# Kernel optimization log

Measured on AMD Instinct MI355X. Metric: run time of the kernel, lower is better.

## Reference

```python
import jax, jax.numpy as jnp
import numpy as np

N_TOKENS = 65536
HIDDEN = 1024
N_EXPERTS = 64
EPS = 1e-12  # matches F.normalize default eps
NEG_BIG = float(jnp.finfo(jnp.bfloat16).max)  # -torch.finfo(bfloat16).max sentinel


def setup_inputs() -> dict:
    key = jax.random.key(0)
    k1, k2 = jax.random.split(key)
    x = jax.random.normal(k1, (N_TOKENS, HIDDEN), dtype=jnp.float32)
    sim_matrix = jax.random.normal(k2, (HIDDEN, N_EXPERTS), dtype=jnp.float32)  # nn.Parameter(randn)
    gates = jnp.zeros((N_EXPERTS,), dtype=jnp.float32)  # nn.Parameter(zeros)
    return {"x": x, "sim_matrix": sim_matrix, "gates": gates}


def _l2norm(v, axis):
    n = jnp.sqrt(jnp.sum(v * v, axis=axis, keepdims=True))
    return v / jnp.maximum(n, EPS)


def reference(x, sim_matrix, gates):
    # cosine-similarity logits: [N, E]
    logits = jnp.matmul(_l2norm(x, -1), _l2norm(sim_matrix, 0))
    thr = jax.nn.sigmoid(gates)                      # [E]
    pre_activation_logits = logits - thr             # [N, E]
    gated = jax.nn.relu(pre_activation_logits)
    # STE: forward hard 0/1, backward identity
    hard = (gated > 0).astype(x.dtype)
    activation_mask = gated + jax.lax.stop_gradient(hard - gated)
    # topk fallback for rows with zero active experts (vectorized scatter)
    inactive = jnp.sum(hard, axis=1) == 0            # [N]
    k_fallback = N_EXPERTS // 2
    _, topk_idx = jax.lax.top_k(logits, k_fallback)  # [N, k]
    rows = jnp.arange(x.shape[0])
    fb = jnp.zeros_like(logits).at[rows[:, None], topk_idx].set(1.0)
    activation_mask = jnp.where(inactive[:, None], fb, activation_mask)
    # masked softmax over active experts
    masked = jnp.where(activation_mask > 0, gated, -NEG_BIG)
    active_expert_probs = jax.nn.softmax(masked, axis=-1)
    return active_expert_probs, pre_activation_logits, activation_mask
```

## Files before the change

### kernel.cpp

```cpp
#include <hip/hip_runtime.h>
#include <math.h>

#define N_TOK   65536
#define HID     1024
#define NEXP    64
#define EPSF    1e-12f

__global__ __launch_bounds__(256) void prep_kernel(const float* __restrict__ sim,
                                                   const float* __restrict__ gates,
                                                   float* __restrict__ ws) {
    __shared__ float partial[4][64];
    int e = threadIdx.x & 63;
    int q = threadIdx.x >> 6;
    float s = 0.f;
    for (int h = q * 256; h < q * 256 + 256; ++h) {
        float v = sim[h * NEXP + e];
        s += v * v;
    }
    partial[q][e] = s;
    __syncthreads();
    if (threadIdx.x < 64) {
        float ss = partial[0][e] + partial[1][e] + partial[2][e] + partial[3][e];
        ws[e] = 1.0f / fmaxf(sqrtf(ss), EPSF);
        ws[64 + e] = 1.0f / (1.0f + expf(-gates[e]));
    }
}

__global__ __launch_bounds__(256) void prep2n_kernel(const float* __restrict__ sim,
                                                     const float* __restrict__ ws_ro,
                                                     float* __restrict__ wn) {
    int idx = blockIdx.x * 256 + threadIdx.x;
    wn[idx] = sim[idx] * ws_ro[idx & 63];
}

__global__ __launch_bounds__(256) void gate_v9_kernel(const float* __restrict__ x,
                                                      const float* __restrict__ wn,
                                                      const float* __restrict__ prep,
                                                      float* __restrict__ out) {
    __shared__ __align__(16) float smem[8960];
    float* ss_part = smem + 8704;

    const int tid  = threadIdx.x;
    const int lane = tid & 63;
    const int wv   = tid >> 6;
    const int tg   = lane >> 3;
    const int eg   = lane & 7;
    const int e0   = eg * 8;
    const int tbase = blockIdx.x * 64;

    float* xsw = smem + wv * 2176;

    const float4* xq4 = (const float4*)(x + (size_t)(tbase + lane) * HID + wv * 256);

    float acc[8][8];
#pragma unroll
    for (int t = 0; t < 8; ++t)
#pragma unroll
        for (int e = 0; e < 8; ++e) acc[t][e] = 0.f;
    float ss = 0.f;

    {
        float4 st[4];
#pragma unroll
        for (int q = 0; q < 4; ++q) st[q] = xq4[q];
#pragma unroll
        for (int q = 0; q < 4; ++q) {
            ss = fmaf(st[q].x, st[q].x, ss);
            ss = fmaf(st[q].y, st[q].y, ss);
            ss = fmaf(st[q].z, st[q].z, ss);
            ss = fmaf(st[q].w, st[q].w, ss);
            xsw[(q * 4 + 0) * 68 + lane] = st[q].x;
            xsw[(q * 4 + 1) * 68 + lane] = st[q].y;
            xsw[(q * 4 + 2) * 68 + lane] = st[q].z;
            xsw[(q * 4 + 3) * 68 + lane] = st[q].w;
        }
    }

#define FMA8x8(XA, XB, WA, WB)                                              \
    do {                                                                    \
        const float xv_[8] = { XA.x, XA.y, XA.z, XA.w, XB.x, XB.y, XB.z, XB.w }; \
        const float wv_[8] = { WA.x, WA.y, WA.z, WA.w, WB.x, WB.y, WB.z, WB.w }; \
        _Pragma("unroll")                                                   \
        for (int t_ = 0; t_ < 8; ++t_)                                      \
            _Pragma("unroll")                                               \
            for (int e_ = 0; e_ < 8; ++e_)                                  \
                acc[t_][e_] = fmaf(xv_[t_], wv_[e_], acc[t_][e_]);          \
    } while (0)

#pragma unroll 1
    for (int c = 0; c < 16; ++c) {
        float4 st[4];
        if (c < 15) {
#pragma unroll
            for (int q = 0; q < 4; ++q) st[q] = xq4[(c + 1) * 4 + q];
        }

        const float* xb = xsw + (c & 1) * 1088;
        const float* wbase = wn + (size_t)(wv * 256 + c * 16) * NEXP + e0;

        float4 a0 = *(const float4*)(wbase);
        float4 b0 = *(const float4*)(wbase + 4);
        float4 a1 = *(const float4*)(wbase + 64);
        float4 b1 = *(const float4*)(wbase + 68);

#pragma unroll 4
        for (int k = 0; k < 16; k += 2) {
            float4 na0, nb0, na1, nb1;
            if (k + 2 < 16) {
                na0 = *(const float4*)(wbase + (k + 2) * 64);
                nb0 = *(const float4*)(wbase + (k + 2) * 64 + 4);
                na1 = *(const float4*)(wbase + (k + 3) * 64);
                nb1 = *(const float4*)(wbase + (k + 3) * 64 + 4);
            }
            const float4 xa0 = *(const float4*)&xb[k * 68 + tg * 8];
            const float4 xb0 = *(const float4*)&xb[k * 68 + tg * 8 + 4];
            const float4 xa1 = *(const float4*)&xb[(k + 1) * 68 + tg * 8];
            const float4 xb1 = *(const float4*)&xb[(k + 1) * 68 + tg * 8 + 4];
            FMA8x8(xa0, xb0, a0, b0);
            FMA8x8(xa1, xb1, a1, b1);
            a0 = na0; b0 = nb0; a1 = na1; b1 = nb1;
        }

        if (c < 15) {
            float* xn = xsw + ((c + 1) & 1) * 1088;
#pragma unroll
            for (int q = 0; q < 4; ++q) {
                ss = fmaf(st[q].x, st[q].x, ss);
                ss = fmaf(st[q].y, st[q].y, ss);
                ss = fmaf(st[q].z, st[q].z, ss);
                ss = fmaf(st[q].w, st[q].w, ss);
                xn[(q * 4 + 0) * 68 + lane] = st[q].x;
                xn[(q * 4 + 1) * 68 + lane] = st[q].y;
                xn[(q * 4 + 2) * 68 + lane] = st[q].z;
                xn[(q * 4 + 3) * 68 + lane] = st[q].w;
            }
        }
    }
#undef FMA8x8

    ss_part[wv * 64 + lane] = ss;
    __syncthreads();

    if (wv < 2) {
        float* reg = smem + wv * 4352;
#pragma unroll
        for (int j = 0; j < 8; ++j) {
            float* p = &reg[(tg * 8 + j) * 68 + e0];
            *(float4*)(p)     = make_float4(acc[j][0], acc[j][1], acc[j][2], acc[j][3]);
            *(float4*)(p + 4) = make_float4(acc[j][4], acc[j][5], acc[j][6], acc[j][7]);
        }
    }
    __syncthreads();
    if (wv >= 2) {
        float* reg = smem + (wv - 2) * 4352;
#pragma unroll
        for (int j = 0; j < 8; ++j) {
            float* p = &reg[(tg * 8 + j) * 68 + e0];
            float4 p0 = *(const float4*)(p);
            float4 p1 = *(const float4*)(p + 4);
            p0.x += acc[j][0]; p0.y += acc[j][1]; p0.z += acc[j][2]; p0.w += acc[j][3];
            p1.x += acc[j][4]; p1.y += acc[j][5]; p1.z += acc[j][6]; p1.w += acc[j][7];
            *(float4*)(p)     = p0;
            *(float4*)(p + 4) = p1;
        }
    }
    __syncthreads();

    float thr[8];
#pragma unroll
    for (int i = 0; i < 8; ++i) thr[i] = prep[64 + e0 + i];

    const size_t out_pre  = (size_t)N_TOK * NEXP;
    const size_t out_mask = 2 * (size_t)N_TOK * NEXP;
    const float* regA = smem;
    const float* regB = smem + 4352;

#pragma unroll
    for (int j = 0; j < 2; ++j) {
        const int tl = wv * 16 + tg * 2 + j;
        const int t  = tbase + tl;
        const float sst = (ss_part[tl] + ss_part[64 + tl])
                        + (ss_part[128 + tl] + ss_part[192 + tl]);
        const float inv = 1.0f / fmaxf(sqrtf(sst), EPSF);

        float4 aA0 = *(const float4*)&regA[tl * 68 + e0];
        float4 aA1 = *(const float4*)&regA[tl * 68 + e0 + 4];
        float4 aB0 = *(const float4*)&regB[tl * 68 + e0];
        float4 aB1 = *(const float4*)&regB[tl * 68 + e0 + 4];
        float logit[8] = { (aA0.x + aB0.x) * inv, (aA0.y + aB0.y) * inv,
                           (aA0.z + aB0.z) * inv, (aA0.w + aB0.w) * inv,
                           (aA1.x + aB1.x) * inv, (aA1.y + aB1.y) * inv,
                           (aA1.z + aB1.z) * inv, (aA1.w + aB1.w) * inv };
        float pre[8], gated[8];
        int active[8];
        int myact = 0;
#pragma unroll
        for (int i = 0; i < 8; ++i) {
            pre[i]   = logit[i] - thr[i];
            gated[i] = fmaxf(pre[i], 0.f);
            active[i] = pre[i] > 0.f;
            myact += active[i];
        }
        int rowact = myact;
        rowact += __shfl_xor(rowact, 1, 8);
        rowact += __shfl_xor(rowact, 2, 8);
        rowact += __shfl_xor(rowact, 4, 8);

        float probs[8], mask[8];
        if (rowact > 0) {
            float m = -INFINITY;
#pragma unroll
            for (int i = 0; i < 8; ++i) m = fmaxf(m, active[i] ? gated[i] : -INFINITY);
            m = fmaxf(m, __shfl_xor(m, 1, 8));
            m = fmaxf(m, __shfl_xor(m, 2, 8));
            m = fmaxf(m, __shfl_xor(m, 4, 8));
            float s = 0.f;
#pragma unroll
            for (int i = 0; i < 8; ++i) {
                float ev = active[i] ? expf(gated[i] - m) : 0.f;
                probs[i] = ev; s += ev;
            }
            s += __shfl_xor(s, 1, 8);
            s += __shfl_xor(s, 2, 8);
            s += __shfl_xor(s, 4, 8);
            float rs = 1.0f / s;
#pragma unroll
            for (int i = 0; i < 8; ++i) {
                probs[i] *= rs;
                mask[i] = active[i] ? 1.f : 0.f;
            }
        } else {
            unsigned key[8];
#pragma unroll
            for (int i = 0; i < 8; ++i) {
                unsigned u = __float_as_uint(logit[i]);
                key[i] = (u & 0x80000000u) ? ~u : (u | 0x80000000u);
            }
            unsigned cand = 0u;
            for (int bit = 31; bit >= 0; --bit) {
                unsigned test = cand | (1u << bit);
                int c = 0;
#pragma unroll
                for (int i = 0; i < 8; ++i) c += (key[i] >= test);
                c += __shfl_xor(c, 1, 8);
                c += __shfl_xor(c, 2, 8);
                c += __shfl_xor(c, 4, 8);
                if (c >= 32) cand = test;
            }
            int cgt = 0;
#pragma unroll
            for (int i = 0; i < 8; ++i) cgt += (key[i] > cand);
            cgt += __shfl_xor(cgt, 1, 8);
            cgt += __shfl_xor(cgt, 2, 8);
            cgt += __shfl_xor(cgt, 4, 8);
            int need_eq = 32 - cgt;

            int eqc = 0;
#pragma unroll
            for (int i = 0; i < 8; ++i) eqc += (key[i] == cand);
            int scan = eqc, tmp;
            tmp = __shfl_up(scan, 1, 8); if (eg >= 1) scan += tmp;
            tmp = __shfl_up(scan, 2, 8); if (eg >= 2) scan += tmp;
            tmp = __shfl_up(scan, 4, 8); if (eg >= 4) scan += tmp;
            int run = scan - eqc;
#pragma unroll
            for (int i = 0; i < 8; ++i) {
                int sel = (key[i] > cand) || ((key[i] == cand) && (run < need_eq));
                run += (key[i] == cand);
                mask[i]  = sel ? 1.f : 0.f;
                probs[i] = sel ? 0.03125f : 0.f;
            }
        }

        const size_t row = (size_t)t * NEXP + e0;
        *(float4*)&out[row]                = make_float4(probs[0], probs[1], probs[2], probs[3]);
        *(float4*)&out[row + 4]            = make_float4(probs[4], probs[5], probs[6], probs[7]);
        *(float4*)&out[out_pre + row]      = make_float4(pre[0], pre[1], pre[2], pre[3]);
        *(float4*)&out[out_pre + row + 4]  = make_float4(pre[4], pre[5], pre[6], pre[7]);
        *(float4*)&out[out_mask + row]     = make_float4(mask[0], mask[1], mask[2], mask[3]);
        *(float4*)&out[out_mask + row + 4] = make_float4(mask[4], mask[5], mask[6], mask[7]);
    }
}

#define TOKB    128
#define KC      64
#define XPAD    65

__global__ __launch_bounds__(256) void gate_kernel_fb(const float* __restrict__ x,
                                                      const float* __restrict__ sim,
                                                      const float* __restrict__ prep,
                                                      float* __restrict__ out) {
    __shared__ float x_lds[TOKB][XPAD];
    __shared__ float w_lds[KC][NEXP];
    __shared__ float ss_lds[TOKB];
    __shared__ float invcol[NEXP];
    __shared__ float thr_s[NEXP];

    const int tid = threadIdx.x;
    const int base_t = blockIdx.x * TOKB;

    if (tid < NEXP) { invcol[tid] = prep[tid]; thr_s[tid] = prep[64 + tid]; }
    if (tid < TOKB) ss_lds[tid] = 0.f;

    const int g_e = tid & 7;
    const int g_t = tid >> 3;
    const int e0 = g_e * 8;
    const int t0 = g_t * 4;

    const int lt = tid >> 4;
    const int lk = (tid & 15) * 4;

    float acc[4][8];
#pragma unroll
    for (int j = 0; j < 4; ++j)
#pragma unroll
        for (int i = 0; i < 8; ++i) acc[j][i] = 0.f;

    for (int kc = 0; kc < HID; kc += KC) {
        __syncthreads();
#pragma unroll
        for (int it = 0; it < 4; ++it) {
            int flat4 = it * 256 + tid;
            int k = flat4 >> 4;
            int e = (flat4 & 15) * 4;
            float4 v = *(const float4*)&sim[(size_t)(kc + k) * NEXP + e];
            v.x *= invcol[e]; v.y *= invcol[e + 1]; v.z *= invcol[e + 2]; v.w *= invcol[e + 3];
            *(float4*)&w_lds[k][e] = v;
        }
#pragma unroll
        for (int it = 0; it < 8; ++it) {
            int t = it * 16 + lt;
            float4 v = *(const float4*)&x[(size_t)(base_t + t) * HID + kc + lk];
            x_lds[t][lk + 0] = v.x; x_lds[t][lk + 1] = v.y;
            x_lds[t][lk + 2] = v.z; x_lds[t][lk + 3] = v.w;
            float s4 = v.x * v.x + v.y * v.y + v.z * v.z + v.w * v.w;
            s4 += __shfl_xor(s4, 1, 16);
            s4 += __shfl_xor(s4, 2, 16);
            s4 += __shfl_xor(s4, 4, 16);
            s4 += __shfl_xor(s4, 8, 16);
            if ((tid & 15) == 0) ss_lds[t] += s4;
        }
        __syncthreads();
#pragma unroll 8
        for (int k = 0; k < KC; ++k) {
            float x0 = x_lds[t0 + 0][k];
            float x1 = x_lds[t0 + 1][k];
            float x2 = x_lds[t0 + 2][k];
            float x3 = x_lds[t0 + 3][k];
            float4 w0 = *(const float4*)&w_lds[k][e0];
            float4 w1 = *(const float4*)&w_lds[k][e0 + 4];
            float wv[8] = { w0.x, w0.y, w0.z, w0.w, w1.x, w1.y, w1.z, w1.w };
#pragma unroll
            for (int i = 0; i < 8; ++i) {
                acc[0][i] += x0 * wv[i];
                acc[1][i] += x1 * wv[i];
                acc[2][i] += x2 * wv[i];
                acc[3][i] += x3 * wv[i];
            }
        }
    }

    const size_t out_pre  = (size_t)N_TOK * NEXP;
    const size_t out_mask = 2 * (size_t)N_TOK * NEXP;

#pragma unroll
    for (int j = 0; j < 4; ++j) {
        int t = t0 + j;
        float inv = 1.0f / fmaxf(sqrtf(ss_lds[t]), EPSF);
        float logit[8], pre[8], gated[8];
        int active[8];
        int myact = 0;
#pragma unroll
        for (int i = 0; i < 8; ++i) {
            logit[i] = acc[j][i] * inv;
            pre[i]   = logit[i] - thr_s[e0 + i];
            gated[i] = fmaxf(pre[i], 0.f);
            active[i] = pre[i] > 0.f;
            myact += active[i];
        }
        int rowact = myact;
        rowact += __shfl_xor(rowact, 1, 8);
        rowact += __shfl_xor(rowact, 2, 8);
        rowact += __shfl_xor(rowact, 4, 8);

        float probs[8], mask[8];
        if (rowact > 0) {
            float m = -INFINITY;
#pragma unroll
            for (int i = 0; i < 8; ++i) m = fmaxf(m, active[i] ? gated[i] : -INFINITY);
            m = fmaxf(m, __shfl_xor(m, 1, 8));
            m = fmaxf(m, __shfl_xor(m, 2, 8));
            m = fmaxf(m, __shfl_xor(m, 4, 8));
            float s = 0.f;
#pragma unroll
            for (int i = 0; i < 8; ++i) {
                float ev = active[i] ? expf(gated[i] - m) : 0.f;
                probs[i] = ev; s += ev;
            }
            s += __shfl_xor(s, 1, 8);
            s += __shfl_xor(s, 2, 8);
            s += __shfl_xor(s, 4, 8);
            float rs = 1.0f / s;
#pragma unroll
            for (int i = 0; i < 8; ++i) {
                probs[i] *= rs;
                mask[i] = active[i] ? 1.f : 0.f;
            }
        } else {
            unsigned key[8];
#pragma unroll
            for (int i = 0; i < 8; ++i) {
                unsigned u = __float_as_uint(logit[i]);
                key[i] = (u & 0x80000000u) ? ~u : (u | 0x80000000u);
            }
            unsigned cand = 0u;
            for (int bit = 31; bit >= 0; --bit) {
                unsigned test = cand | (1u << bit);
                int c = 0;
#pragma unroll
                for (int i = 0; i < 8; ++i) c += (key[i] >= test);
                c += __shfl_xor(c, 1, 8);
                c += __shfl_xor(c, 2, 8);
                c += __shfl_xor(c, 4, 8);
                if (c >= 32) cand = test;
            }
            int cgt = 0;
#pragma unroll
            for (int i = 0; i < 8; ++i) cgt += (key[i] > cand);
            cgt += __shfl_xor(cgt, 1, 8);
            cgt += __shfl_xor(cgt, 2, 8);
            cgt += __shfl_xor(cgt, 4, 8);
            int need_eq = 32 - cgt;

            int eqc = 0;
#pragma unroll
            for (int i = 0; i < 8; ++i) eqc += (key[i] == cand);
            int scan = eqc, tmp;
            tmp = __shfl_up(scan, 1, 8); if (g_e >= 1) scan += tmp;
            tmp = __shfl_up(scan, 2, 8); if (g_e >= 2) scan += tmp;
            tmp = __shfl_up(scan, 4, 8); if (g_e >= 4) scan += tmp;
            int run = scan - eqc;
#pragma unroll
            for (int i = 0; i < 8; ++i) {
                int sel = (key[i] > cand) || ((key[i] == cand) && (run < need_eq));
                run += (key[i] == cand);
                mask[i]  = sel ? 1.f : 0.f;
                probs[i] = sel ? 0.03125f : 0.f;
            }
        }

        size_t row = (size_t)(base_t + t) * NEXP + e0;
        *(float4*)&out[row]                = make_float4(probs[0], probs[1], probs[2], probs[3]);
        *(float4*)&out[row + 4]            = make_float4(probs[4], probs[5], probs[6], probs[7]);
        *(float4*)&out[out_pre + row]      = make_float4(pre[0], pre[1], pre[2], pre[3]);
        *(float4*)&out[out_pre + row + 4]  = make_float4(pre[4], pre[5], pre[6], pre[7]);
        *(float4*)&out[out_mask + row]     = make_float4(mask[0], mask[1], mask[2], mask[3]);
        *(float4*)&out[out_mask + row + 4] = make_float4(mask[4], mask[5], mask[6], mask[7]);
    }
}

extern "C" void kernel_launch(void* const* d_in, const int* in_sizes, int n_in,
                              void* d_out, int out_size, void* d_ws, size_t ws_size,
                              hipStream_t stream) {
    (void)in_sizes; (void)n_in; (void)out_size;
    const float* x     = (const float*)d_in[0];
    const float* sim   = (const float*)d_in[1];
    const float* gates = (const float*)d_in[2];
    float* out = (float*)d_out;
    float* ws  = (float*)d_ws;

    hipLaunchKernelGGL(prep_kernel, dim3(1), dim3(256), 0, stream, sim, gates, ws);

    const size_t need = 512 + (size_t)HID * NEXP * sizeof(float);
    if (ws_size >= need) {
        float* wn = ws + 128;
        hipLaunchKernelGGL(prep2n_kernel, dim3(HID * NEXP / 256), dim3(256), 0, stream,
                           sim, ws, wn);
        hipLaunchKernelGGL(gate_v9_kernel, dim3(N_TOK / 64), dim3(256), 0, stream,
                           x, wn, ws, out);
    } else {
        hipLaunchKernelGGL(gate_kernel_fb, dim3(N_TOK / TOKB), dim3(256), 0, stream,
                           x, sim, ws, out);
    }
}
```

Baseline: 174.7 us.

## Stage normalized weights through per-wave LDS double buffer alongside x tiles

Each wave now loads its slice of the normalized weight matrix cooperatively into a double-buffered LDS region, in 8-row chunks next to the x tile, instead of every lane pulling float4 weights straight from global or cache. The K loop becomes 32 chunks of 8 rows with software prefetch of both x and weights into registers. The aim is to cut redundant global and L1 weight traffic so the FMA loop is fed from LDS. The partial-sum reduction buffer stride also changes from 68 to 65 to change its bank mapping, which leaves float4 LDS accesses misaligned and adds more LDS load and store work per chunk.

```diff
diff --git a/kernel.cpp b/kernel.cpp
--- a/kernel.cpp
+++ b/kernel.cpp
@@ -33,12 +33,12 @@
     wn[idx] = sim[idx] * ws_ro[idx & 63];
 }
 
-__global__ __launch_bounds__(256) void gate_v9_kernel(const float* __restrict__ x,
-                                                      const float* __restrict__ wn,
-                                                      const float* __restrict__ prep,
-                                                      float* __restrict__ out) {
-    __shared__ __align__(16) float smem[8960];
-    float* ss_part = smem + 8704;
+__global__ __launch_bounds__(256) void gate_v10_kernel(const float* __restrict__ x,
+                                                       const float* __restrict__ wn,
+                                                       const float* __restrict__ prep,
+                                                       float* __restrict__ out) {
+    __shared__ __align__(16) float smem[8704];
+    float* ss_part = smem + 8448;
 
     const int tid  = threadIdx.x;
     const int lane = tid & 63;
@@ -47,10 +47,11 @@
     const int eg   = lane & 7;
     const int e0   = eg * 8;
     const int tbase = blockIdx.x * 64;
-
-    float* xsw = smem + wv * 2176;
-
-    const float4* xq4 = (const float4*)(x + (size_t)(tbase + lane) * HID + wv * 256);
+    const int kbase = wv * 256;
+
+    float* xsw = smem + wv * 2112;
+
+    const float4* xq4 = (const float4*)(x + (size_t)(tbase + lane) * HID + kbase);
 
     float acc[8][8];
 #pragma unroll
@@ -60,20 +61,17 @@
     float ss = 0.f;
 
     {
-        float4 st[4];
-#pragma unroll
-        for (int q = 0; q < 4; ++q) st[q] = xq4[q];
-#pragma unroll
-        for (int q = 0; q < 4; ++q) {
-            ss = fmaf(st[q].x, st[q].x, ss);
-            ss = fmaf(st[q].y, st[q].y, ss);
-            ss = fmaf(st[q].z, st[q].z, ss);
-            ss = fmaf(st[q].w, st[q].w, ss);
-            xsw[(q * 4 + 0) * 68 + lane] = st[q].x;
-            xsw[(q * 4 + 1) * 68 + lane] = st[q].y;
-            xsw[(q * 4 + 2) * 68 + lane] = st[q].z;
-            xsw[(q * 4 + 3) * 68 + lane] = st[q].w;
-        }
+        float4 f0 = xq4[0], f1 = xq4[1];
+        const float4* wq4 = (const float4*)(wn + (size_t)kbase * NEXP) + lane * 2;
+        float4 w0 = wq4[0], w1 = wq4[1];
+        const float a[8] = { f0.x, f0.y, f0.z, f0.w, f1.x, f1.y, f1.z, f1.w };
+#pragma unroll
+        for (int i = 0; i < 8; ++i) {
+            ss = fmaf(a[i], a[i], ss);
+            xsw[i * 68 + lane] = a[i];
+        }
+        *(float4*)&xsw[1088 + lane * 8]     = w0;
+        *(float4*)&xsw[1088 + lane * 8 + 4] = w1;
     }
 
 #define FMA8x8(XA, XB, WA, WB)                                              \
@@ -88,52 +86,40 @@
     } while (0)
 
 #pragma unroll 1
-    for (int c = 0; c < 16; ++c) {
-        float4 st[4];
-        if (c < 15) {
-#pragma unroll
-            for (int q = 0; q < 4; ++q) st[q] = xq4[(c + 1) * 4 + q];
-        }
-
-        const float* xb = xsw + (c & 1) * 1088;
-        const float* wbase = wn + (size_t)(wv * 256 + c * 16) * NEXP + e0;
-
-        float4 a0 = *(const float4*)(wbase);
-        float4 b0 = *(const float4*)(wbase + 4);
-        float4 a1 = *(const float4*)(wbase + 64);
-        float4 b1 = *(const float4*)(wbase + 68);
-
-#pragma unroll 4
-        for (int k = 0; k < 16; k += 2) {
-            float4 na0, nb0, na1, nb1;
-            if (k + 2 < 16) {
-                na0 = *(const float4*)(wbase + (k + 2) * 64);
-                nb0 = *(const float4*)(wbase + (k + 2) * 64 + 4);
-                na1 = *(const float4*)(wbase + (k + 3) * 64);
-                nb1 = *(const float4*)(wbase + (k + 3) * 64 + 4);
-            }
-            const float4 xa0 = *(const float4*)&xb[k * 68 + tg * 8];
-            const float4 xb0 = *(const float4*)&xb[k * 68 + tg * 8 + 4];
-            const float4 xa1 = *(const float4*)&xb[(k + 1) * 68 + tg * 8];
-            const float4 xb1 = *(const float4*)&xb[(k + 1) * 68 + tg * 8 + 4];
-            FMA8x8(xa0, xb0, a0, b0);
-            FMA8x8(xa1, xb1, a1, b1);
-            a0 = na0; b0 = nb0; a1 = na1; b1 = nb1;
-        }
-
-        if (c < 15) {
-            float* xn = xsw + ((c + 1) & 1) * 1088;
-#pragma unroll
-            for (int q = 0; q < 4; ++q) {
-                ss = fmaf(st[q].x, st[q].x, ss);
-                ss = fmaf(st[q].y, st[q].y, ss);
-                ss = fmaf(st[q].z, st[q].z, ss);
-                ss = fmaf(st[q].w, st[q].w, ss);
-                xn[(q * 4 + 0) * 68 + lane] = st[q].x;
-                xn[(q * 4 + 1) * 68 + lane] = st[q].y;
-                xn[(q * 4 + 2) * 68 + lane] = st[q].z;
-                xn[(q * 4 + 3) * 68 + lane] = st[q].w;
-            }
+    for (int c = 0; c < 32; ++c) {
+        float4 sx0, sx1, sw0, sw1;
+        if (c < 31) {
+            sx0 = xq4[(c + 1) * 2];
+            sx1 = xq4[(c + 1) * 2 + 1];
+            const float4* wq4 = (const float4*)(wn + (size_t)(kbase + (c + 1) * 8) * NEXP)
+                              + lane * 2;
+            sw0 = wq4[0];
+            sw1 = wq4[1];
+        }
+
+        const float* xb = xsw + (c & 1) * 544;
+        const float* wb = xsw + 1088 + (c & 1) * 512;
+
+#pragma unroll
+        for (int k = 0; k < 8; ++k) {
+            const float4 xa = *(const float4*)&xb[k * 68 + tg * 8];
+            const float4 xc = *(const float4*)&xb[k * 68 + tg * 8 + 4];
+            const float4 wa = *(const float4*)&wb[k * 64 + e0];
+            const float4 wc = *(const float4*)&wb[k * 64 + e0 + 4];
+            FMA8x8(xa, xc, wa, wc);
+        }
+
+        if (c < 31) {
+            float* xn = xsw + ((c + 1) & 1) * 544;
+            float* wl = xsw + 1088 + ((c + 1) & 1) * 512;
+            const float a[8] = { sx0.x, sx0.y, sx0.z, sx0.w, sx1.x, sx1.y, sx1.z, sx1.w };
+#pragma unroll
+            for (int i = 0; i < 8; ++i) {
+                ss = fmaf(a[i], a[i], ss);
+                xn[i * 68 + lane] = a[i];
+            }
+            *(float4*)&wl[lane * 8]     = sw0;
+            *(float4*)&wl[lane * 8 + 4] = sw1;
         }
     }
 #undef FMA8x8
@@ -142,20 +128,20 @@
     __syncthreads();
 
     if (wv < 2) {
-        float* reg = smem + wv * 4352;
+        float* reg = smem + wv * 4224;
 #pragma unroll
         for (int j = 0; j < 8; ++j) {
-            float* p = &reg[(tg * 8 + j) * 68 + e0];
+            float* p = &reg[(tg * 8 + j) * 65 + e0];
             *(float4*)(p)     = make_float4(acc[j][0], acc[j][1], acc[j][2], acc[j][3]);
             *(float4*)(p + 4) = make_float4(acc[j][4], acc[j][5], acc[j][6], acc[j][7]);
         }
     }
     __syncthreads();
     if (wv >= 2) {
-        float* reg = smem + (wv - 2) * 4352;
+        float* reg = smem + (wv - 2) * 4224;
 #pragma unroll
         for (int j = 0; j < 8; ++j) {
-            float* p = &reg[(tg * 8 + j) * 68 + e0];
+            float* p = &reg[(tg * 8 + j) * 65 + e0];
             float4 p0 = *(const float4*)(p);
             float4 p1 = *(const float4*)(p + 4);
             p0.x += acc[j][0]; p0.y += acc[j][1]; p0.z += acc[j][2]; p0.w += acc[j][3];
@@ -173,7 +159,7 @@
     const size_t out_pre  = (size_t)N_TOK * NEXP;
     const size_t out_mask = 2 * (size_t)N_TOK * NEXP;
     const float* regA = smem;
-    const float* regB = smem + 4352;
+    const float* regB = smem + 4224;
 
 #pragma unroll
     for (int j = 0; j < 2; ++j) {
@@ -183,10 +169,10 @@
                         + (ss_part[128 + tl] + ss_part[192 + tl]);
         const float inv = 1.0f / fmaxf(sqrtf(sst), EPSF);
 
-        float4 aA0 = *(const float4*)&regA[tl * 68 + e0];
-        float4 aA1 = *(const float4*)&regA[tl * 68 + e0 + 4];
-        float4 aB0 = *(const float4*)&regB[tl * 68 + e0];
-        float4 aB1 = *(const float4*)&regB[tl * 68 + e0 + 4];
+        float4 aA0 = *(const float4*)&regA[tl * 65 + e0];
+        float4 aA1 = *(const float4*)&regA[tl * 65 + e0 + 4];
+        float4 aB0 = *(const float4*)&regB[tl * 65 + e0];
+        float4 aB1 = *(const float4*)&regB[tl * 65 + e0 + 4];
         float logit[8] = { (aA0.x + aB0.x) * inv, (aA0.y + aB0.y) * inv,
                            (aA0.z + aB0.z) * inv, (aA0.w + aB0.w) * inv,
                            (aA1.x + aB1.x) * inv, (aA1.y + aB1.y) * inv,
@@ -476,7 +462,7 @@
         float* wn = ws + 128;
         hipLaunchKernelGGL(prep2n_kernel, dim3(HID * NEXP / 256), dim3(256), 0, stream,
                            sim, ws, wn);
-        hipLaunchKernelGGL(gate_v9_kernel, dim3(N_TOK / 64), dim3(256), 0, stream,
+        hipLaunchKernelGGL(gate_v10_kernel, dim3(N_TOK / 64), dim3(256), 0, stream,
                            x, wn, ws, out);
     } else {
         hipLaunchKernelGGL(gate_kernel_fb, dim3(N_TOK / TOKB), dim3(256), 0, stream,
```

Result: faster. 161.5 us (-7.6%).
